# Performance work log

Hardware: AMD Instinct MI355X
Metric: run time of the kernel (lower is better)

## Reference

```python
import jax, jax.numpy as jnp
import numpy as np


def _grid_sample_bilinear(img, grid):
    # img: [N, C, H, W]; grid: [N, Ho, Wo, 2] (x,y) in [-1,1]
    # matches torch.nn.functional.grid_sample(mode='bilinear', padding_mode='zeros', align_corners=False)
    N, C, H, W = img.shape
    Ho, Wo = grid.shape[1], grid.shape[2]
    ix = (grid[..., 0] + 1.0) * (W * 0.5) - 0.5  # unnormalize, align_corners=False
    iy = (grid[..., 1] + 1.0) * (H * 0.5) - 0.5
    x0 = jnp.floor(ix)
    y0 = jnp.floor(iy)
    x1 = x0 + 1.0
    y1 = y0 + 1.0
    wx1 = ix - x0
    wx0 = 1.0 - wx1
    wy1 = iy - y0
    wy0 = 1.0 - wy1
    img_flat = img.reshape(N, C, H * W)

    def corner(xf, yf, w):
        valid = (xf >= 0) & (xf <= W - 1) & (yf >= 0) & (yf <= H - 1)
        xi = jnp.clip(xf.astype(jnp.int32), 0, W - 1)
        yi = jnp.clip(yf.astype(jnp.int32), 0, H - 1)
        idx = (yi * W + xi).reshape(N, 1, Ho * Wo)
        vals = jnp.take_along_axis(img_flat, idx, axis=2)  # [N, C, Ho*Wo]
        wv = (w * valid.astype(img.dtype)).reshape(N, 1, Ho * Wo)
        return vals * wv

    out = (corner(x0, y0, wx0 * wy0) + corner(x1, y0, wx1 * wy0)
           + corner(x0, y1, wx0 * wy1) + corner(x1, y1, wx1 * wy1))
    return out.reshape(N, C, Ho, Wo)


def setup_inputs() -> dict:
    key = jax.random.key(0)
    k1, k2 = jax.random.split(key)
    B, L, C, H, W = 2, 24, 16, 64, 64
    flows = jax.random.normal(k1, (B, L, 2, H, W), dtype=jnp.float32) * 0.01
    images = jax.random.normal(k2, (B, L, C, H, W), dtype=jnp.float32)
    return {"flows": flows, "images": images}


def reference(flows, images):
    B, L, _, H, W = flows.shape
    C = images.shape[2]
    dtype = flows.dtype
    cum_flows = jnp.cumsum(flows.astype(jnp.float32), axis=1).astype(dtype)  # [B,L,2,H,W]
    k_idx, t_idx = np.triu_indices(L)  # all pairs k <= t, N_pairs = L(L+1)/2
    N_pairs = k_idx.size
    # relative flow from frame k to frame t for every pair
    rel = (cum_flows[:, t_idx] - cum_flows[:, k_idx])  # [B, N_pairs, 2, H, W]
    rel = rel.reshape(B * N_pairs, 2, H, W).transpose(0, 2, 3, 1)  # [BN, H, W, 2]
    # pixel-center base grid (align_corners=False convention)
    gy = jnp.linspace(-1.0 + 1.0 / H, 1.0 - 1.0 / H, H, dtype=dtype)
    gx = jnp.linspace(-1.0 + 1.0 / W, 1.0 - 1.0 / W, W, dtype=dtype)
    base = jnp.stack(jnp.meshgrid(gx, gy, indexing='xy'), axis=-1)  # [H, W, 2] (x,y)
    grid = base[None] + rel
    # wrap x coordinate into [-1, 1)
    grid = grid.at[..., 0].set(jnp.remainder(grid[..., 0] + 1.0, 2.0) - 1.0)
    flat_images = images[:, k_idx].reshape(B * N_pairs, C, H, W)
    warped = _grid_sample_bilinear(flat_images, grid)  # [BN, C, H, W]
    targets = (np.arange(B)[:, None] * L + t_idx[None, :]).reshape(-1)
    out = jax.ops.segment_sum(warped, jnp.asarray(targets), num_segments=B * L)
    return out.reshape(B, L, C, H, W)
```

## Files before the change

kernel.cpp:

```cpp
#include <hip/hip_runtime.h>


#define BB 2
#define LL 24
#define CC 16
#define HH 64
#define WW 64
#define HW (HH * WW)

__device__ __forceinline__ void bilin_coords(
    float gxv0, float gyv,
    int& i00, int& i10, int& i01, int& i11,
    float& w00, float& w10, float& w01, float& w11)
{
    const float v = gxv0 + 1.0f;
    float r = v - 2.0f * truncf(v * 0.5f);
    r = (r < 0.0f) ? (r + 2.0f) : r;
    const float gxv = r - 1.0f;

    const float ix = (gxv + 1.0f) * 32.0f - 0.5f;
    const float iy = (gyv + 1.0f) * 32.0f - 0.5f;

    const float x0f = floorf(ix);
    const float y0f = floorf(iy);
    const float x1f = x0f + 1.0f;
    const float y1f = y0f + 1.0f;

    const float wx1 = ix - x0f, wx0 = 1.0f - wx1;
    const float wy1 = iy - y0f, wy0 = 1.0f - wy1;

    const bool vx0 = (x0f >= 0.0f) && (x0f <= 63.0f);
    const bool vx1 = (x1f >= 0.0f) && (x1f <= 63.0f);
    const bool vy0 = (y0f >= 0.0f) && (y0f <= 63.0f);
    const bool vy1 = (y1f >= 0.0f) && (y1f <= 63.0f);

    const int x0 = min(max((int)x0f, 0), WW - 1);
    const int x1 = min(max((int)x1f, 0), WW - 1);
    const int y0 = min(max((int)y0f, 0), HH - 1);
    const int y1 = min(max((int)y1f, 0), HH - 1);

    w00 = (vx0 && vy0) ? (wx0 * wy0) : 0.0f;
    w10 = (vx1 && vy0) ? (wx1 * wy0) : 0.0f;
    w01 = (vx0 && vy1) ? (wx0 * wy1) : 0.0f;
    w11 = (vx1 && vy1) ? (wx1 * wy1) : 0.0f;

    i00 = y0 * WW + x0;
    i10 = y0 * WW + x1;
    i01 = y1 * WW + x0;
    i11 = y1 * WW + x1;
}

__global__ __launch_bounds__(64) void transpose_kernel(
    const float* __restrict__ img, float* __restrict__ imgT)
{
    const int bid = blockIdx.x;
    const int y = bid % HH;
    const int l = (bid / HH) % LL;
    const int b = bid / (HH * LL);
    const int x = threadIdx.x;

    const float* src = img + ((size_t)(b * LL + l) * CC) * HW + y * WW + x;
    float v[CC];
#pragma unroll
    for (int c = 0; c < CC; ++c) v[c] = src[(size_t)c * HW];

    float* dst = imgT + ((size_t)(b * LL + l) * HW + y * WW + x) * CC;
#pragma unroll
    for (int c = 0; c < CC; c += 4)
        *(float4*)(dst + c) = make_float4(v[c], v[c + 1], v[c + 2], v[c + 3]);
}

__global__ __launch_bounds__(64) void gsps_main(
    const float* __restrict__ flows,
    const float* __restrict__ imgT,
    float* __restrict__ out)
{
    const int bid = blockIdx.x;
    const int y_lo = bid & 7;
    const int r1 = bid >> 3;
    const int t = (LL - 1) - (r1 % LL);
    const int r2 = r1 / LL;
    const int y = ((r2 & 7) << 3) | y_lo;
    const int b = r2 >> 3;
    const int x = threadIdx.x;

    const float gx = -0.984375f + (float)x * 0.03125f;
    const float gy = -0.984375f + (float)y * 0.03125f;
    const int pix = y * WW + x;
    const float* fb = flows + (size_t)b * LL * 2 * HW + pix;

    float ctx = 0.0f, cty = 0.0f;
    for (int i = 0; i <= t; ++i) {
        ctx += fb[(size_t)(2 * i) * HW];
        cty += fb[(size_t)(2 * i + 1) * HW];
    }

    float acc[CC];
#pragma unroll
    for (int c = 0; c < CC; ++c) acc[c] = 0.0f;

    const char* pb = (const char*)imgT + (size_t)b * LL * HW * 64;
    float cx = 0.0f, cy = 0.0f;
    float fkx = fb[0], fky = fb[HW];

    for (int k = 0; k <= t; ++k) {
        cx += fkx; cy += fky;
        if (k < t) {
            fkx = fb[(size_t)(2 * (k + 1)) * HW];
            fky = fb[(size_t)(2 * (k + 1) + 1) * HW];
        }

        int i00, i10, i01, i11;
        float w00, w10, w01, w11;
        bilin_coords(gx + (ctx - cx), gy + (cty - cy), i00, i10, i01, i11, w00, w10, w01, w11);

        const char* plane = pb + (size_t)k * (HW * 64);
        const float4* r00 = (const float4*)(plane + (size_t)i00 * 64);
        const float4* r10 = (const float4*)(plane + (size_t)i10 * 64);
        const float4* r01 = (const float4*)(plane + (size_t)i01 * 64);
        const float4* r11 = (const float4*)(plane + (size_t)i11 * 64);

        float4 v00[4], v10[4], v01[4], v11[4];
#pragma unroll
        for (int j = 0; j < 4; ++j) v00[j] = r00[j];
#pragma unroll
        for (int j = 0; j < 4; ++j) v10[j] = r10[j];
#pragma unroll
        for (int j = 0; j < 4; ++j) v01[j] = r01[j];
#pragma unroll
        for (int j = 0; j < 4; ++j) v11[j] = r11[j];

#pragma unroll
        for (int j = 0; j < 4; ++j) {
            acc[4 * j + 0] += v00[j].x * w00 + v10[j].x * w10 + v01[j].x * w01 + v11[j].x * w11;
            acc[4 * j + 1] += v00[j].y * w00 + v10[j].y * w10 + v01[j].y * w01 + v11[j].y * w11;
            acc[4 * j + 2] += v00[j].z * w00 + v10[j].z * w10 + v01[j].z * w01 + v11[j].z * w11;
            acc[4 * j + 3] += v00[j].w * w00 + v10[j].w * w10 + v01[j].w * w01 + v11[j].w * w11;
        }
    }

    float* o = out + ((size_t)(b * LL + t) * CC) * HW + pix;
#pragma unroll
    for (int c = 0; c < CC; ++c) o[(size_t)c * HW] = acc[c];
}

__global__ __launch_bounds__(256) void gsps_direct(
    const float* __restrict__ flows,
    const float* __restrict__ images,
    float* __restrict__ out)
{
    const int bid = blockIdx.x;
    const int t = (LL - 1) - (bid % LL);
    const int y = (bid / LL) % HH;
    const int b = bid / (LL * HH);
    const int x = threadIdx.x & 63;
    const int wave = threadIdx.x >> 6;
    const int cw = wave * 4;

    const float gx = -0.984375f + (float)x * 0.03125f;
    const float gy = -0.984375f + (float)y * 0.03125f;
    const int pix = y * WW + x;
    const float* fb = flows + (size_t)b * LL * 2 * HW + pix;

    float ctx = 0.0f, cty = 0.0f;
    for (int i = 0; i <= t; ++i) {
        ctx += fb[(size_t)(i * 2) * HW];
        cty += fb[(size_t)(i * 2 + 1) * HW];
    }

    float acc[4] = {0.0f, 0.0f, 0.0f, 0.0f};
    float cx = 0.0f, cy = 0.0f;
    float fxk = fb[0];
    float fyk = fb[HW];

    for (int k = 0; k <= t; ++k) {
        cx += fxk; cy += fyk;
        if (k < t) {
            fxk = fb[(size_t)((k + 1) * 2) * HW];
            fyk = fb[(size_t)((k + 1) * 2 + 1) * HW];
        }

        int i00, i10, i01, i11;
        float w00, w10, w01, w11;
        bilin_coords(gx + (ctx - cx), gy + (cty - cy), i00, i10, i01, i11, w00, w10, w01, w11);

        const float* img = images + (((size_t)(b * LL + k) * CC) + cw) * HW;
#pragma unroll
        for (int c = 0; c < 4; ++c) {
            const float* pc = img + (size_t)c * HW;
            acc[c] += pc[i00] * w00 + pc[i10] * w10 + pc[i01] * w01 + pc[i11] * w11;
        }
    }

    float* o = out + ((size_t)(b * LL + t) * CC + cw) * HW + pix;
#pragma unroll
    for (int c = 0; c < 4; ++c) o[(size_t)c * HW] = acc[c];
}

extern "C" void kernel_launch(void* const* d_in, const int* in_sizes, int n_in,
                              void* d_out, int out_size, void* d_ws, size_t ws_size,
                              hipStream_t stream) {
    const float* flows  = (const float*)d_in[0];
    const float* images = (const float*)d_in[1];
    float* out = (float*)d_out;

    const size_t needT = (size_t)BB * LL * CC * HW * sizeof(float);
    const int nblk = BB * LL * HH;

    if (ws_size >= needT) {
        float* imgT = (float*)d_ws;
        transpose_kernel<<<nblk, 64, 0, stream>>>(images, imgT);
        gsps_main<<<nblk, 64, 0, stream>>>(flows, imgT, out);
    } else {
        gsps_direct<<<nblk, 256, 0, stream>>>(flows, images, out);
    }
}
```

Before: 166.9 us.

## Stage source image rows in LDS shared across target frames per block

The main kernel now runs one block per (batch, row, residue class q), with six wavefronts each handling target frame t = q + 4w. For every source frame k, the block computes the band of rows its bilinear samples touch and loads those rows cooperatively into swizzled LDS. All waves then gather the four corners from LDS instead of global memory. If the band exceeds 14 rows, it falls back to direct global gathers. This replaces repeated scattered global reads across t with shared staged reads, at the cost of two barriers per k, idle waves for inactive t, and fewer blocks overall.

Result: slower. 236.8 us (+41.8%).

```diff
diff --git a/kernel.cpp b/kernel.cpp
--- a/kernel.cpp
+++ b/kernel.cpp
@@ -7,10 +7,17 @@
 #define HH 64
 #define WW 64
 #define HW (HH * WW)
+#define NW 6
+#define CAP 14
+#define ROWB 4096
+
+__device__ __forceinline__ int swzb(int z) {
+    return z ^ (((z >> 7) & 3) << 4);
+}
 
 __device__ __forceinline__ void bilin_coords(
     float gxv0, float gyv,
-    int& i00, int& i10, int& i01, int& i11,
+    int& x0c, int& x1c, int& y0c, int& y1c,
     float& w00, float& w10, float& w01, float& w11)
 {
     const float v = gxv0 + 1.0f;
@@ -34,20 +41,15 @@
     const bool vy0 = (y0f >= 0.0f) && (y0f <= 63.0f);
     const bool vy1 = (y1f >= 0.0f) && (y1f <= 63.0f);
 
-    const int x0 = min(max((int)x0f, 0), WW - 1);
-    const int x1 = min(max((int)x1f, 0), WW - 1);
-    const int y0 = min(max((int)y0f, 0), HH - 1);
-    const int y1 = min(max((int)y1f, 0), HH - 1);
+    x0c = min(max((int)x0f, 0), WW - 1);
+    x1c = min(max((int)x1f, 0), WW - 1);
+    y0c = min(max((int)y0f, 0), HH - 1);
+    y1c = min(max((int)y1f, 0), HH - 1);
 
     w00 = (vx0 && vy0) ? (wx0 * wy0) : 0.0f;
     w10 = (vx1 && vy0) ? (wx1 * wy0) : 0.0f;
     w01 = (vx0 && vy1) ? (wx0 * wy1) : 0.0f;
     w11 = (vx1 && vy1) ? (wx1 * wy1) : 0.0f;
-
-    i00 = y0 * WW + x0;
-    i10 = y0 * WW + x1;
-    i01 = y1 * WW + x0;
-    i11 = y1 * WW + x1;
 }
 
 __global__ __launch_bounds__(64) void transpose_kernel(
@@ -70,23 +72,29 @@
         *(float4*)(dst + c) = make_float4(v[c], v[c + 1], v[c + 2], v[c + 3]);
 }
 
-__global__ __launch_bounds__(64) void gsps_main(
+__global__ __launch_bounds__(NW * 64) void gsps_lds(
     const float* __restrict__ flows,
     const float* __restrict__ imgT,
     float* __restrict__ out)
 {
+    __shared__ float4 buf4[CAP * 256];
+    __shared__ int bandW[NW];
+
     const int bid = blockIdx.x;
-    const int y_lo = bid & 7;
-    const int r1 = bid >> 3;
-    const int t = (LL - 1) - (r1 % LL);
-    const int r2 = r1 / LL;
-    const int y = ((r2 & 7) << 3) | y_lo;
-    const int b = r2 >> 3;
-    const int x = threadIdx.x;
-
-    const float gx = -0.984375f + (float)x * 0.03125f;
+    const int y_hi = bid & 7;
+    int u = bid >> 3;
+    const int y_lo = u & 7; u >>= 3;
+    const int q = u & 3;
+    const int b = u >> 2;
+    const int y = (y_hi << 3) | y_lo;
+    const int lane = threadIdx.x & 63;
+    const int w = threadIdx.x >> 6;
+    const int t = q + 4 * w;
+    const int kmax = q + 20;
+
+    const float gx = -0.984375f + (float)lane * 0.03125f;
     const float gy = -0.984375f + (float)y * 0.03125f;
-    const int pix = y * WW + x;
+    const int pix = y * WW + lane;
     const float* fb = flows + (size_t)b * LL * 2 * HW + pix;
 
     float ctx = 0.0f, cty = 0.0f;
@@ -99,43 +107,111 @@
 #pragma unroll
     for (int c = 0; c < CC; ++c) acc[c] = 0.0f;
 
-    const char* pb = (const char*)imgT + (size_t)b * LL * HW * 64;
     float cx = 0.0f, cy = 0.0f;
     float fkx = fb[0], fky = fb[HW];
 
-    for (int k = 0; k <= t; ++k) {
+    for (int k = 0; k <= kmax; ++k) {
         cx += fkx; cy += fky;
-        if (k < t) {
+        if (k < kmax) {
             fkx = fb[(size_t)(2 * (k + 1)) * HW];
             fky = fb[(size_t)(2 * (k + 1) + 1) * HW];
         }
 
-        int i00, i10, i01, i11;
-        float w00, w10, w01, w11;
-        bilin_coords(gx + (ctx - cx), gy + (cty - cy), i00, i10, i01, i11, w00, w10, w01, w11);
-
-        const char* plane = pb + (size_t)k * (HW * 64);
-        const float4* r00 = (const float4*)(plane + (size_t)i00 * 64);
-        const float4* r10 = (const float4*)(plane + (size_t)i10 * 64);
-        const float4* r01 = (const float4*)(plane + (size_t)i01 * 64);
-        const float4* r11 = (const float4*)(plane + (size_t)i11 * 64);
-
-        float4 v00[4], v10[4], v01[4], v11[4];
-#pragma unroll
-        for (int j = 0; j < 4; ++j) v00[j] = r00[j];
-#pragma unroll
-        for (int j = 0; j < 4; ++j) v10[j] = r10[j];
-#pragma unroll
-        for (int j = 0; j < 4; ++j) v01[j] = r01[j];
-#pragma unroll
-        for (int j = 0; j < 4; ++j) v11[j] = r11[j];
-
-#pragma unroll
-        for (int j = 0; j < 4; ++j) {
-            acc[4 * j + 0] += v00[j].x * w00 + v10[j].x * w10 + v01[j].x * w01 + v11[j].x * w11;
-            acc[4 * j + 1] += v00[j].y * w00 + v10[j].y * w10 + v01[j].y * w01 + v11[j].y * w11;
-            acc[4 * j + 2] += v00[j].z * w00 + v10[j].z * w10 + v01[j].z * w01 + v11[j].z * w11;
-            acc[4 * j + 3] += v00[j].w * w00 + v10[j].w * w10 + v01[j].w * w01 + v11[j].w * w11;
+        const bool act = (t >= k);
+        int x0c = 0, x1c = 0, y0c = 0, y1c = 0;
+        float w00 = 0.f, w10 = 0.f, w01 = 0.f, w11 = 0.f;
+        if (act)
+            bilin_coords(gx + (ctx - cx), gy + (cty - cy),
+                         x0c, x1c, y0c, y1c, w00, w10, w01, w11);
+
+        int ymn = act ? y0c : 64;
+        int ymx = act ? y1c : -1;
+#pragma unroll
+        for (int m = 1; m < 64; m <<= 1) {
+            ymn = min(ymn, __shfl_xor(ymn, m));
+            ymx = max(ymx, __shfl_xor(ymx, m));
+        }
+        if (lane == 0) bandW[w] = (ymn << 8) | (ymx + 1);
+        __syncthreads();
+
+        int lo = 64, hx = 0;
+#pragma unroll
+        for (int ww = 0; ww < NW; ++ww) {
+            const int bv = bandW[ww];
+            lo = min(lo, bv >> 8);
+            hx = max(hx, bv & 255);
+        }
+        const int nrows = hx - lo;
+        const bool fbk = nrows > CAP;
+
+        const float* plane = imgT + (size_t)(b * LL + k) * (HW * CC);
+
+        const int r0g = lo + w, r1g = r0g + NW, r2g = r1g + NW;
+        const bool h0 = !fbk && (r0g < lo + nrows);
+        const bool h1 = !fbk && (r1g < lo + nrows);
+        const bool h2 = !fbk && (r2g < lo + nrows);
+        float4 rv0[4], rv1[4], rv2[4];
+        if (h0) { const float* rb = plane + (size_t)r0g * 1024;
+#pragma unroll
+            for (int rr = 0; rr < 4; ++rr) rv0[rr] = *(const float4*)(rb + rr * 256 + lane * 4); }
+        if (h1) { const float* rb = plane + (size_t)r1g * 1024;
+#pragma unroll
+            for (int rr = 0; rr < 4; ++rr) rv1[rr] = *(const float4*)(rb + rr * 256 + lane * 4); }
+        if (h2) { const float* rb = plane + (size_t)r2g * 1024;
+#pragma unroll
+            for (int rr = 0; rr < 4; ++rr) rv2[rr] = *(const float4*)(rb + rr * 256 + lane * 4); }
+
+        if (h0) {
+#pragma unroll
+            for (int rr = 0; rr < 4; ++rr)
+                *(float4*)((char*)buf4 + (r0g - lo) * ROWB + swzb(lane * 16 + rr * 1024)) = rv0[rr];
+        }
+        if (h1) {
+#pragma unroll
+            for (int rr = 0; rr < 4; ++rr)
+                *(float4*)((char*)buf4 + (r1g - lo) * ROWB + swzb(lane * 16 + rr * 1024)) = rv1[rr];
+        }
+        if (h2) {
+#pragma unroll
+            for (int rr = 0; rr < 4; ++rr)
+                *(float4*)((char*)buf4 + (r2g - lo) * ROWB + swzb(lane * 16 + rr * 1024)) = rv2[rr];
+        }
+        __syncthreads();
+
+        if (act) {
+            if (!fbk) {
+                const char* lb = (const char*)buf4;
+                const int rA = (y0c - lo) * ROWB;
+                const int rB = (y1c - lo) * ROWB;
+                const int zx0 = x0c * 64, zx1 = x1c * 64;
+#pragma unroll
+                for (int j = 0; j < 4; ++j) {
+                    const float4 v00 = *(const float4*)(lb + rA + swzb(zx0 + j * 16));
+                    const float4 v10 = *(const float4*)(lb + rA + swzb(zx1 + j * 16));
+                    const float4 v01 = *(const float4*)(lb + rB + swzb(zx0 + j * 16));
+                    const float4 v11 = *(const float4*)(lb + rB + swzb(zx1 + j * 16));
+                    acc[4 * j + 0] += v00.x * w00 + v10.x * w10 + v01.x * w01 + v11.x * w11;
+                    acc[4 * j + 1] += v00.y * w00 + v10.y * w10 + v01.y * w01 + v11.y * w11;
+                    acc[4 * j + 2] += v00.z * w00 + v10.z * w10 + v01.z * w01 + v11.z * w11;
+                    acc[4 * j + 3] += v00.w * w00 + v10.w * w10 + v01.w * w01 + v11.w * w11;
+                }
+            } else {
+                const float* p00 = plane + (size_t)(y0c * WW + x0c) * CC;
+                const float* p10 = plane + (size_t)(y0c * WW + x1c) * CC;
+                const float* p01 = plane + (size_t)(y1c * WW + x0c) * CC;
+                const float* p11 = plane + (size_t)(y1c * WW + x1c) * CC;
+#pragma unroll
+                for (int j = 0; j < 4; ++j) {
+                    const float4 v00 = *(const float4*)(p00 + j * 4);
+                    const float4 v10 = *(const float4*)(p10 + j * 4);
+                    const float4 v01 = *(const float4*)(p01 + j * 4);
+                    const float4 v11 = *(const float4*)(p11 + j * 4);
+                    acc[4 * j + 0] += v00.x * w00 + v10.x * w10 + v01.x * w01 + v11.x * w11;
+                    acc[4 * j + 1] += v00.y * w00 + v10.y * w10 + v01.y * w01 + v11.y * w11;
+                    acc[4 * j + 2] += v00.z * w00 + v10.z * w10 + v01.z * w01 + v11.z * w11;
+                    acc[4 * j + 3] += v00.w * w00 + v10.w * w10 + v01.w * w01 + v11.w * w11;
+                }
+            }
         }
     }
 
@@ -170,8 +246,7 @@
 
     float acc[4] = {0.0f, 0.0f, 0.0f, 0.0f};
     float cx = 0.0f, cy = 0.0f;
-    float fxk = fb[0];
-    float fyk = fb[HW];
+    float fxk = fb[0], fyk = fb[HW];
 
     for (int k = 0; k <= t; ++k) {
         cx += fxk; cy += fyk;
@@ -179,16 +254,15 @@
             fxk = fb[(size_t)((k + 1) * 2) * HW];
             fyk = fb[(size_t)((k + 1) * 2 + 1) * HW];
         }
-
-        int i00, i10, i01, i11;
-        float w00, w10, w01, w11;
-        bilin_coords(gx + (ctx - cx), gy + (cty - cy), i00, i10, i01, i11, w00, w10, w01, w11);
+        int x0c, x1c, y0c, y1c; float w00, w10, w01, w11;
+        bilin_coords(gx + (ctx - cx), gy + (cty - cy), x0c, x1c, y0c, y1c, w00, w10, w01, w11);
 
         const float* img = images + (((size_t)(b * LL + k) * CC) + cw) * HW;
 #pragma unroll
         for (int c = 0; c < 4; ++c) {
             const float* pc = img + (size_t)c * HW;
-            acc[c] += pc[i00] * w00 + pc[i10] * w10 + pc[i01] * w01 + pc[i11] * w11;
+            acc[c] += pc[y0c * WW + x0c] * w00 + pc[y0c * WW + x1c] * w10
+                    + pc[y1c * WW + x0c] * w01 + pc[y1c * WW + x1c] * w11;
         }
     }
 
@@ -205,13 +279,12 @@
     float* out = (float*)d_out;
 
     const size_t needT = (size_t)BB * LL * CC * HW * sizeof(float);
-    const int nblk = BB * LL * HH;
 
     if (ws_size >= needT) {
         float* imgT = (float*)d_ws;
-        transpose_kernel<<<nblk, 64, 0, stream>>>(images, imgT);
-        gsps_main<<<nblk, 64, 0, stream>>>(flows, imgT, out);
+        transpose_kernel<<<BB * LL * HH, 64, 0, stream>>>(images, imgT);
+        gsps_lds<<<BB * 4 * HH, NW * 64, 0, stream>>>(flows, imgT, out);
     } else {
-        gsps_direct<<<nblk, 256, 0, stream>>>(flows, images, out);
-    }
-}
+        gsps_direct<<<BB * LL * HH, 256, 0, stream>>>(flows, images, out);
+    }
+}
```
